# Kernel tuning notes

Hardware: AMD Instinct MI355X
Metric: run time of the kernel (lower is better)

Reference implementation:

```python
import jax, jax.numpy as jnp
import numpy as np
import math

# ---- dims ----
B, N, IN_DIM = 4, 512, 128
D, H, DH = 256, 8, 32          # embed_dim, heads, dim_head
L = 8                           # performer depth
M = int(DH * math.log(DH))      # 110 FAVOR+ random features (performer_pytorch default)
HID = 256                       # lstm hidden
FF = 4 * D
EPS_K = 1e-4                    # kernel feature eps
EPS_D = 1e-6                    # denominator eps


def setup_inputs() -> dict:
    key = jax.random.key(0)
    ks = iter(jax.random.split(key, 40))
    def nrm(shape, s=0.02):
        return jax.random.normal(next(ks), shape, dtype=jnp.float32) * s
    z = lambda shape: jnp.zeros(shape, jnp.float32)
    o = lambda shape: jnp.ones(shape, jnp.float32)
    return {
        "x": jax.random.normal(next(ks), (B, N, IN_DIM), dtype=jnp.float32),
        # input projection
        "Win_w": nrm((D, IN_DIM)), "Win_b": z((D,)),
        # performer layers (stacked over L)
        "ln1_w": o((L, D)), "ln1_b": z((L, D)),
        "Wq": nrm((L, D, D)), "bq": z((L, D)),
        "Wk": nrm((L, D, D)), "bk": z((L, D)),
        "Wv": nrm((L, D, D)), "bv": z((L, D)),
        "Wo": nrm((L, D, D)), "bo": z((L, D)),
        "proj": jax.random.normal(next(ks), (L, M, DH), dtype=jnp.float32),  # FAVOR+ projections
        "ln2_w": o((L, D)), "ln2_b": z((L, D)),
        "Wff1": nrm((L, FF, D)), "bff1": z((L, FF)),
        "Wff2": nrm((L, D, FF)), "bff2": z((L, D)),
        # BiLSTM: layer0 input D, layers1-2 input 2*HID; [dir] / [layer,dir] stacks
        "Wih0": nrm((2, 4 * HID, D)), "Whh0": nrm((2, 4 * HID, HID)), "b0": z((2, 2, 4 * HID)),
        "Wih12": nrm((2, 2, 4 * HID, 2 * HID)), "Whh12": nrm((2, 2, 4 * HID, HID)), "b12": z((2, 2, 2, 4 * HID)),
        # final head
        "fc_w": nrm((1, 2 * HID)), "fc_b": z((1,)),
    }


def layer_norm(x, w, b):
    mu = jnp.mean(x, -1, keepdims=True)
    var = jnp.mean((x - mu) ** 2, -1, keepdims=True)
    return (x - mu) * jax.lax.rsqrt(var + 1e-5) * w + b


def softmax_features(x, proj, is_query):
    # FAVOR+ positive softmax-kernel features. x:[b,h,n,dh], proj:[m,dh]
    xd = x * (DH ** -0.25)
    dd = jnp.einsum('bhnd,md->bhnm', xd, proj)
    diag = 0.5 * jnp.sum(xd * xd, -1)[..., None]            # [b,h,n,1]
    if is_query:
        stab = jnp.max(dd, axis=-1, keepdims=True)
    else:
        stab = jnp.max(dd, axis=(-2, -1), keepdims=True)
    return (M ** -0.5) * (jnp.exp(dd - diag - stab) + EPS_K)


def causal_linear_attention(qp, kp, v):
    # qp,kp:[b,h,n,m], v:[b,h,n,dv] -> [b,h,n,dv]; cumulative-sum causal form
    k_cum = jnp.cumsum(kp, axis=2)
    d_inv = 1.0 / (jnp.einsum('bhnm,bhnm->bhn', qp, k_cum) + EPS_D)
    ctx = jnp.cumsum(jnp.einsum('bhnm,bhnd->bhnmd', kp, v), axis=2)
    return jnp.einsum('bhnmd,bhnm,bhn->bhnd', ctx, qp, d_inv)


def performer_block(x, p):
    (lw1, lb1, wq, bq_, wk, bk_, wv, bv_, wo, bo_, pr, lw2, lb2, w1, b1, w2, b2) = p
    b, n = x.shape[0], x.shape[1]
    y = layer_norm(x, lw1, lb1)
    sh = lambda t: t.reshape(b, n, H, DH).transpose(0, 2, 1, 3)
    q = sh(y @ wq.T + bq_)
    k = sh(y @ wk.T + bk_)
    v = sh(y @ wv.T + bv_)
    qp = softmax_features(q, pr, True)
    kp = softmax_features(k, pr, False)
    o = causal_linear_attention(qp, kp, v)
    o = o.transpose(0, 2, 1, 3).reshape(b, n, D)
    x = x + o @ wo.T + bo_
    y = layer_norm(x, lw2, lb2)
    x = x + jax.nn.gelu(y @ w1.T + b1, approximate=False) @ w2.T + b2
    return x, None


def lstm_dir(x, wih, whh, b, reverse):
    # x:[B,N,in] -> hs:[B,N,HID]; torch gate order i,f,g,o
    xs = jnp.flip(x, 1) if reverse else x
    gi = xs.transpose(1, 0, 2) @ wih.T + b                  # [N,B,4H] precomputed input part
    def step(carry, g_in):
        h, c = carry
        g = g_in + h @ whh.T
        i, f, gg, oo = jnp.split(g, 4, axis=-1)
        c = jax.nn.sigmoid(f) * c + jax.nn.sigmoid(i) * jnp.tanh(gg)
        h = jax.nn.sigmoid(oo) * jnp.tanh(c)
        return (h, c), h
    h0 = jnp.zeros((x.shape[0], HID), x.dtype)
    _, hs = jax.lax.scan(step, (h0, h0), gi)
    hs = hs.transpose(1, 0, 2)
    return jnp.flip(hs, 1) if reverse else hs


def bilstm_layer(x, wih, whh, b):
    fwd = lstm_dir(x, wih[0], whh[0], b[0, 0] + b[0, 1], False)
    bwd = lstm_dir(x, wih[1], whh[1], b[1, 0] + b[1, 1], True)
    return jnp.concatenate([fwd, bwd], -1)


def reference(x, Win_w, Win_b, ln1_w, ln1_b, Wq, bq, Wk, bk, Wv, bv, Wo, bo, proj,
              ln2_w, ln2_b, Wff1, bff1, Wff2, bff2,
              Wih0, Whh0, b0, Wih12, Whh12, b12, fc_w, fc_b):
    h = x @ Win_w.T + Win_b
    params = (ln1_w, ln1_b, Wq, bq, Wk, bk, Wv, bv, Wo, bo, proj, ln2_w, ln2_b, Wff1, bff1, Wff2, bff2)
    h, _ = jax.lax.scan(performer_block, h, params)       # 8 performer layers
    # dropout is identity at eval
    h = bilstm_layer(h, Wih0, Whh0, b0)
    h = bilstm_layer(h, Wih12[0], Whh12[0], b12[0])
    h = bilstm_layer(h, Wih12[1], Whh12[1], b12[1])
    return h[:, -1, :] @ fc_w.T + fc_b                    # [B,1]
```

## Files before the change

### kernel.cpp

```cpp
#include <hip/hip_runtime.h>
#include <math.h>

#define B_    4
#define N_    512
#define D_    256
#define H_    8
#define DH_   32
#define M_    110
#define MP_   112
#define FF_   1024
#define HID_  256
#define ROWS_ 2048
#define CHUNK 32
#define NCH   16

#define OFF_H      0u
#define OFF_Y      524288u
#define OFF_Q      1048576u
#define OFF_K      1572864u
#define OFF_V      2097152u
#define OFF_O      2621440u
#define OFF_FF     3145728u
#define OFF_QP     5242880u
#define OFF_KP     7077888u
#define OFF_S      8912896u
#define OFF_MB     9437184u
#define OFF_P      10747904u
#define OFF_KSUM   12582912u
#define OFF_PK     12640256u
#define OFF_DIAG   12697600u
#define OFF_KMAX   12713984u

#define SCALE_X 0.42044820762685725f
#define SCALE_M 0.09534625892455924f

__device__ __forceinline__ float sigmoidf_(float x){ return 1.0f/(1.0f+expf(-x)); }
__device__ __forceinline__ float geluf_(float x){ return 0.5f*x*(1.0f+erff(x*0.70710678118654752f)); }
__device__ __forceinline__ unsigned encf_(float x){ unsigned u=__float_as_uint(x); return (u&0x80000000u)?~u:(u|0x80000000u); }
__device__ __forceinline__ float decf_(unsigned u){ return (u&0x80000000u)?__uint_as_float(u&0x7fffffffu):__uint_as_float(~u); }

typedef unsigned u32x4_ __attribute__((ext_vector_type(4)));

__device__ __forceinline__ u32x4_ ld4_l2_(const unsigned* p){
  u32x4_ v;
  asm volatile("global_load_dwordx4 %0, %1, off sc0\n\ts_waitcnt vmcnt(0)"
               : "=v"(v) : "v"(p));
  return v;
}
__device__ __forceinline__ u32x4_ ld4_far_(const unsigned* p){
  u32x4_ v;
  asm volatile("global_load_dwordx4 %0, %1, off sc0 sc1\n\ts_waitcnt vmcnt(0)"
               : "=v"(v) : "v"(p));
  return v;
}

__global__ __launch_bounds__(256) void gemm_k(
    const float* __restrict__ A, const float* __restrict__ W,
    const float* __restrict__ b1, const float* __restrict__ b2,
    const float* __restrict__ R, float* __restrict__ C,
    int M, int N, int K, int act)
{
  __shared__ float As[16][72];
  __shared__ float Ws[16][72];
  const int tid = threadIdx.x;
  const int tx = tid & 15, ty = tid >> 4;
  const int i0 = blockIdx.y * 64, j0 = blockIdx.x * 64;
  const int lr = tid >> 2, lc = (tid & 3) << 2;
  float acc[4][4] = {};
  for (int k0 = 0; k0 < K; k0 += 16) {
    float4 a4 = *(const float4*)(A + (size_t)(i0 + lr) * K + k0 + lc);
    float4 w4 = *(const float4*)(W + (size_t)(j0 + lr) * K + k0 + lc);
    __syncthreads();
    As[lc+0][lr]=a4.x; As[lc+1][lr]=a4.y; As[lc+2][lr]=a4.z; As[lc+3][lr]=a4.w;
    Ws[lc+0][lr]=w4.x; Ws[lc+1][lr]=w4.y; Ws[lc+2][lr]=w4.z; Ws[lc+3][lr]=w4.w;
    __syncthreads();
    #pragma unroll
    for (int kk = 0; kk < 16; kk++) {
      float4 av = *(const float4*)&As[kk][ty*4];
      float4 wv = *(const float4*)&Ws[kk][tx*4];
      acc[0][0] += av.x*wv.x; acc[0][1] += av.x*wv.y; acc[0][2] += av.x*wv.z; acc[0][3] += av.x*wv.w;
      acc[1][0] += av.y*wv.x; acc[1][1] += av.y*wv.y; acc[1][2] += av.y*wv.z; acc[1][3] += av.y*wv.w;
      acc[2][0] += av.z*wv.x; acc[2][1] += av.z*wv.y; acc[2][2] += av.z*wv.z; acc[2][3] += av.z*wv.w;
      acc[3][0] += av.w*wv.x; acc[3][1] += av.w*wv.y; acc[3][2] += av.w*wv.z; acc[3][3] += av.w*wv.w;
    }
  }
  #pragma unroll
  for (int ii = 0; ii < 4; ii++) {
    int gi_ = i0 + ty*4 + ii;
    #pragma unroll
    for (int jj = 0; jj < 4; jj++) {
      int gj = j0 + tx*4 + jj;
      float v = acc[ii][jj];
      if (b1) v += b1[gj];
      if (b2) v += b2[gj];
      if (act) v = geluf_(v);
      if (R) v += R[(size_t)gi_ * N + gj];
      C[(size_t)gi_ * N + gj] = v;
    }
  }
}

__global__ __launch_bounds__(256) void gemm3_k(
    const float* __restrict__ A,
    const float* __restrict__ W0, const float* __restrict__ W1, const float* __restrict__ W2,
    const float* __restrict__ c0_, const float* __restrict__ c1_, const float* __restrict__ c2_,
    float* __restrict__ O0, float* __restrict__ O1, float* __restrict__ O2)
{
  const int which = blockIdx.x >> 2;
  const float* W  = which == 0 ? W0 : which == 1 ? W1 : W2;
  const float* bb = which == 0 ? c0_ : which == 1 ? c1_ : c2_;
  float* C        = which == 0 ? O0 : which == 1 ? O1 : O2;
  __shared__ float As[16][72];
  __shared__ float Ws[16][72];
  const int tid = threadIdx.x;
  const int tx = tid & 15, ty = tid >> 4;
  const int i0 = blockIdx.y * 64, j0 = (blockIdx.x & 3) * 64;
  const int lr = tid >> 2, lc = (tid & 3) << 2;
  float acc[4][4] = {};
  for (int k0 = 0; k0 < 256; k0 += 16) {
    float4 a4 = *(const float4*)(A + (size_t)(i0 + lr) * 256 + k0 + lc);
    float4 w4 = *(const float4*)(W + (size_t)(j0 + lr) * 256 + k0 + lc);
    __syncthreads();
    As[lc+0][lr]=a4.x; As[lc+1][lr]=a4.y; As[lc+2][lr]=a4.z; As[lc+3][lr]=a4.w;
    Ws[lc+0][lr]=w4.x; Ws[lc+1][lr]=w4.y; Ws[lc+2][lr]=w4.z; Ws[lc+3][lr]=w4.w;
    __syncthreads();
    #pragma unroll
    for (int kk = 0; kk < 16; kk++) {
      float4 av = *(const float4*)&As[kk][ty*4];
      float4 wv = *(const float4*)&Ws[kk][tx*4];
      acc[0][0] += av.x*wv.x; acc[0][1] += av.x*wv.y; acc[0][2] += av.x*wv.z; acc[0][3] += av.x*wv.w;
      acc[1][0] += av.y*wv.x; acc[1][1] += av.y*wv.y; acc[1][2] += av.y*wv.z; acc[1][3] += av.y*wv.w;
      acc[2][0] += av.z*wv.x; acc[2][1] += av.z*wv.y; acc[2][2] += av.z*wv.z; acc[2][3] += av.z*wv.w;
      acc[3][0] += av.w*wv.x; acc[3][1] += av.w*wv.y; acc[3][2] += av.w*wv.z; acc[3][3] += av.w*wv.w;
    }
  }
  #pragma unroll
  for (int ii = 0; ii < 4; ii++) {
    int gi_ = i0 + ty*4 + ii;
    #pragma unroll
    for (int jj = 0; jj < 4; jj++) {
      int gj = j0 + tx*4 + jj;
      C[(size_t)gi_ * 256 + gj] = acc[ii][jj] + bb[gj];
    }
  }
}

__global__ __launch_bounds__(256) void ln_k(const float* __restrict__ x, const float* __restrict__ w,
                                            const float* __restrict__ b, float* __restrict__ y)
{
  const int row = blockIdx.x, t = threadIdx.x;
  float v = x[(size_t)row * 256 + t];
  float s = v;
  #pragma unroll
  for (int o = 32; o >= 1; o >>= 1) s += __shfl_xor(s, o, 64);
  __shared__ float w1_[4], w2_[4];
  const int wid = t >> 6, lane = t & 63;
  if (lane == 0) w1_[wid] = s;
  __syncthreads();
  float mu = (w1_[0] + w1_[1] + w1_[2] + w1_[3]) * (1.0f/256.0f);
  float d = v - mu;
  float s2 = d * d;
  #pragma unroll
  for (int o = 32; o >= 1; o >>= 1) s2 += __shfl_xor(s2, o, 64);
  if (lane == 0) w2_[wid] = s2;
  __syncthreads();
  float var = (w2_[0] + w2_[1] + w2_[2] + w2_[3]) * (1.0f/256.0f);
  y[(size_t)row * 256 + t] = d * (1.0f / sqrtf(var + 1e-5f)) * w[t] + b[t];
}

__global__ __launch_bounds__(256) void featq_k(const float* __restrict__ q, const float* __restrict__ proj,
                                               float* __restrict__ qp)
{
  const int wid = threadIdx.x >> 6, lane = threadIdx.x & 63;
  const int p = blockIdx.x * 4 + wid;
  const int bh = p >> 9, n = p & 511;
  const int b = bh >> 3, h = bh & 7;
  __shared__ float xs[4][32];
  const float* qrow = q + ((size_t)(b * N_ + n)) * D_ + h * DH_;
  if (lane < 32) xs[wid][lane] = qrow[lane] * SCALE_X;
  __syncthreads();
  float diag = 0.f;
  #pragma unroll
  for (int d = 0; d < 32; d++) { float xv = xs[wid][d]; diag += xv * xv; }
  diag *= 0.5f;
  const int m0 = lane, m1 = 64 + lane;
  float dd0 = 0.f, dd1 = -INFINITY;
  #pragma unroll
  for (int d = 0; d < 32; d++) dd0 += xs[wid][d] * proj[m0 * 32 + d];
  if (m1 < M_) {
    float a = 0.f;
    #pragma unroll
    for (int d = 0; d < 32; d++) a += xs[wid][d] * proj[m1 * 32 + d];
    dd1 = a;
  }
  float mx = fmaxf(dd0, dd1);
  #pragma unroll
  for (int o = 32; o >= 1; o >>= 1) mx = fmaxf(mx, __shfl_xor(mx, o, 64));
  float* out = qp + (size_t)p * MP_;
  out[m0] = SCALE_M * (expf(dd0 - diag - mx) + 1e-4f);
  if (m1 < M_)        out[m1] = SCALE_M * (expf(dd1 - diag - mx) + 1e-4f);
  else if (m1 < MP_)  out[m1] = 0.f;
}

__global__ __launch_bounds__(256) void featk1_k(const float* __restrict__ k, const float* __restrict__ proj,
                                                float* __restrict__ kpraw, float* __restrict__ diagb,
                                                unsigned* __restrict__ kmax)
{
  const int wid = threadIdx.x >> 6, lane = threadIdx.x & 63;
  const int p = blockIdx.x * 4 + wid;
  const int bh = p >> 9, n = p & 511;
  const int b = bh >> 3, h = bh & 7;
  __shared__ float xs[4][32];
  const float* krow = k + ((size_t)(b * N_ + n)) * D_ + h * DH_;
  if (lane < 32) xs[wid][lane] = krow[lane] * SCALE_X;
  __syncthreads();
  float diag = 0.f;
  #pragma unroll
  for (int d = 0; d < 32; d++) { float xv = xs[wid][d]; diag += xv * xv; }
  diag *= 0.5f;
  const int m0 = lane, m1 = 64 + lane;
  float dd0 = 0.f, dd1 = -INFINITY;
  #pragma unroll
  for (int d = 0; d < 32; d++) dd0 += xs[wid][d] * proj[m0 * 32 + d];
  if (m1 < M_) {
    float a = 0.f;
    #pragma unroll
    for (int d = 0; d < 32; d++) a += xs[wid][d] * proj[m1 * 32 + d];
    dd1 = a;
  }
  float mx = fmaxf(dd0, dd1);
  #pragma unroll
  for (int o = 32; o >= 1; o >>= 1) mx = fmaxf(mx, __shfl_xor(mx, o, 64));
  float* out = kpraw + (size_t)p * MP_;
  out[m0] = dd0;
  if (m1 < M_) out[m1] = dd1;
  if (lane == 0) { diagb[p] = diag; atomicMax(kmax + bh, encf_(mx)); }
}

__global__ __launch_bounds__(256) void featk2_k(float* __restrict__ kp, const float* __restrict__ diagb,
                                                const unsigned* __restrict__ kmax)
{
  const int idx = blockIdx.x * 256 + threadIdx.x;
  const int p = idx / MP_, m = idx - p * MP_;
  const int bh = p >> 9;
  float v = 0.f;
  if (m < M_) v = SCALE_M * (expf(kp[idx] - diagb[p] - decf_(kmax[bh])) + 1e-4f);
  kp[idx] = v;
}

__global__ __launch_bounds__(256) void csum_k(const float* __restrict__ kp, const float* __restrict__ v,
                                              float* __restrict__ S, float* __restrict__ ksum)
{
  const int bh = blockIdx.x >> 4, c = blockIdx.x & 15;
  const int b = bh >> 3, h = bh & 7;
  __shared__ float kpc[CHUNK * MP_];
  __shared__ float vc[CHUNK][DH_];
  const float* kpbase = kp + ((size_t)bh * N_ + c * CHUNK) * MP_;
  for (int f = threadIdx.x; f < CHUNK * MP_; f += 256) kpc[f] = kpbase[f];
  for (int f = threadIdx.x; f < CHUNK * DH_; f += 256) {
    int i = f >> 5, d = f & 31;
    vc[i][d] = v[((size_t)(b * N_ + c * CHUNK + i)) * D_ + h * DH_ + d];
  }
  __syncthreads();
  const int d = threadIdx.x & 31, mg = threadIdx.x >> 5;
  float Sa[14] = {};
  for (int i = 0; i < CHUNK; i++) {
    float vv = vc[i][d];
    #pragma unroll
    for (int j = 0; j < 14; j++) Sa[j] += kpc[i * MP_ + mg * 14 + j] * vv;
  }
  float* Sout = S + (((size_t)blockIdx.x) * MP_ + mg * 14) * DH_ + d;
  #pragma unroll
  for (int j = 0; j < 14; j++) Sout[(size_t)j * DH_] = Sa[j];
  if (threadIdx.x < MP_) {
    float s = 0.f;
    for (int i = 0; i < CHUNK; i++) s += kpc[i * MP_ + threadIdx.x];
    ksum[(size_t)blockIdx.x * MP_ + threadIdx.x] = s;
  }
}

__global__ __launch_bounds__(256) void cpref_k(const float* __restrict__ S, const float* __restrict__ ksum,
                                               float* __restrict__ P, float* __restrict__ pk)
{
  const int bh = blockIdx.x;
  const int d = threadIdx.x & 31, mg = threadIdx.x >> 5;
  float run[14] = {};
  for (int c = 0; c < NCH; c++) {
    size_t base = (((size_t)(bh * NCH + c)) * MP_ + mg * 14) * DH_ + d;
    #pragma unroll
    for (int j = 0; j < 14; j++) { P[base + (size_t)j * DH_] = run[j]; run[j] += S[base + (size_t)j * DH_]; }
  }
  if (threadIdx.x < MP_) {
    float r = 0.f;
    for (int c = 0; c < NCH; c++) {
      size_t o = (size_t)(bh * NCH + c) * MP_ + threadIdx.x;
      pk[o] = r; r += ksum[o];
    }
  }
}

__global__ __launch_bounds__(256, 1) void attn_k(const float* __restrict__ qp, const float* __restrict__ kp,
                                                 const float* __restrict__ v, const float* __restrict__ P,
                                                 const float* __restrict__ pk, float* __restrict__ o)
{
  const int bh = blockIdx.x >> 4, c = blockIdx.x & 15;
  const int b = bh >> 3, h = bh & 7;
  __shared__ float qpc[CHUNK * 113];
  __shared__ float kpc[CHUNK * 113];
  __shared__ float vc[CHUNK][DH_];
  __shared__ float Pl[MP_ * DH_];
  __shared__ float pkl[MP_];
  __shared__ float Al[CHUNK * 33];
  __shared__ float den[CHUNK];
  const int t = threadIdx.x;
  const float* qbase = qp + ((size_t)bh * N_ + c * CHUNK) * MP_;
  const float* kbase = kp + ((size_t)bh * N_ + c * CHUNK) * MP_;
  for (int f = t; f < CHUNK * MP_; f += 256) {
    int i = f / MP_, m = f - i * MP_;
    qpc[i * 113 + m] = qbase[f];
    kpc[i * 113 + m] = kbase[f];
  }
  for (int f = t; f < CHUNK * DH_; f += 256) {
    int i = f >> 5, d = f & 31;
    vc[i][d] = v[((size_t)(b * N_ + c * CHUNK + i)) * D_ + h * DH_ + d];
  }
  for (int f = t; f < MP_ * DH_; f += 256) Pl[f] = P[((size_t)blockIdx.x) * MP_ * DH_ + f];
  if (t < MP_) pkl[t] = pk[(size_t)blockIdx.x * MP_ + t];
  __syncthreads();
  {
    const int ti = t >> 4, tj = t & 15;
    float a00 = 0.f, a01 = 0.f, a10 = 0.f, a11 = 0.f;
    for (int m = 0; m < MP_; m++) {
      float q0 = qpc[(ti*2+0)*113 + m], q1 = qpc[(ti*2+1)*113 + m];
      float k0 = kpc[(tj*2+0)*113 + m], k1 = kpc[(tj*2+1)*113 + m];
      a00 += q0*k0; a01 += q0*k1; a10 += q1*k0; a11 += q1*k1;
    }
    const int i0_ = ti*2, j0_ = tj*2;
    Al[(i0_  )*33 + j0_  ] = (j0_   <= i0_  ) ? a00 : 0.f;
    Al[(i0_  )*33 + j0_+1] = (j0_+1 <= i0_  ) ? a01 : 0.f;
    Al[(i0_+1)*33 + j0_  ] = (j0_   <= i0_+1) ? a10 : 0.f;
    Al[(i0_+1)*33 + j0_+1] = (j0_+1 <= i0_+1) ? a11 : 0.f;
  }
  __syncthreads();
  if (t < CHUNK) {
    const int i = t; float s = 0.f;
    for (int m = 0; m < MP_; m++) s += qpc[i*113 + m] * pkl[m];
    for (int j = 0; j <= i; j++) s += Al[i*33 + j];
    den[i] = 1.0f / (s + 1e-6f);
  }
  __syncthreads();
  {
    const int d = t & 31, ig = t >> 5;
    float Pd[MP_];
    #pragma unroll
    for (int m = 0; m < MP_; m++) Pd[m] = Pl[m * DH_ + d];
    float vd[CHUNK];
    #pragma unroll
    for (int j = 0; j < CHUNK; j++) vd[j] = vc[j][d];
    for (int r = 0; r < 4; r++) {
      const int i = ig * 4 + r;
      float acc = 0.f;
      #pragma unroll
      for (int m = 0; m < MP_; m++) acc += qpc[i*113 + m] * Pd[m];
      #pragma unroll
      for (int j = 0; j < CHUNK; j++) acc += Al[i*33 + j] * vd[j];
      o[((size_t)(b * N_ + c * CHUNK + i)) * D_ + h * DH_ + d] = acc * den[i];
    }
  }
}

__global__ __launch_bounds__(256, 1) void rec_k(
    const float* __restrict__ gi, const float* __restrict__ whh,
    float* __restrict__ hs, float* __restrict__ hx)
{
  const int bid = blockIdx.x;
  if ((bid & 7) > 1) return;
  const int dir = bid & 7;
  const int s = bid >> 3;
  if (s >= 16) return;
  const int t = threadIdx.x;

  const float* giD = gi + (size_t)dir * 2097152;
  const float* whD = whh + (size_t)dir * 262144;
  float* hxD = hx + (size_t)dir * 524288;

  __shared__ __align__(16) float h_sh[4][256];
  __shared__ __align__(16) float red[64 * 33];
  __shared__ __align__(16) float gsh[64 * 5];

  __builtin_amdgcn_fence(__ATOMIC_ACQUIRE, "agent");

  const int rg = t & 31, kq = t >> 5;
  float4 w4[2][8];
  #pragma unroll
  for (int rr = 0; rr < 2; rr++) {
    const int rho = rg * 2 + rr;
    const int grow = (rho >> 4) * 256 + s * 16 + (rho & 15);
    const float4* src = (const float4*)(whD + (size_t)grow * 256 + kq * 32);
    #pragma unroll
    for (int q = 0; q < 8; q++) w4[rr][q] = src[q];
  }

  const int rho2 = t & 63, b2 = t >> 6;
  const float* pgi = giD + (size_t)b2 * 524288 + (size_t)((rho2 >> 4) * 256 + s * 16 + (rho2 & 15));

  ((float4*)h_sh)[t] = make_float4(0.f, 0.f, 0.f, 0.f);
  float c0 = 0.f;
  __syncthreads();

  int n = dir ? 511 : 0;
  float gnext = pgi[(size_t)n * 1024];

  for (int step = 0; step < 512; step++) {
    const float gval = gnext;
    const int n2 = dir ? (510 - step) : (step + 1);
    if (step < 511) gnext = pgi[(size_t)n2 * 1024];

    float acc[2][4] = {};
    #pragma unroll
    for (int q = 0; q < 8; q++) {
      float4 h0 = *(const float4*)&h_sh[0][kq * 32 + q * 4];
      float4 h1 = *(const float4*)&h_sh[1][kq * 32 + q * 4];
      float4 h2 = *(const float4*)&h_sh[2][kq * 32 + q * 4];
      float4 h3 = *(const float4*)&h_sh[3][kq * 32 + q * 4];
      #pragma unroll
      for (int rr = 0; rr < 2; rr++) {
        float4 w = w4[rr][q];
        acc[rr][0] += w.x*h0.x + w.y*h0.y + w.z*h0.z + w.w*h0.w;
        acc[rr][1] += w.x*h1.x + w.y*h1.y + w.z*h1.z + w.w*h1.w;
        acc[rr][2] += w.x*h2.x + w.y*h2.y + w.z*h2.z + w.w*h2.w;
        acc[rr][3] += w.x*h3.x + w.y*h3.y + w.z*h3.z + w.w*h3.w;
      }
    }
    #pragma unroll
    for (int rr = 0; rr < 2; rr++)
      #pragma unroll
      for (int b = 0; b < 4; b++)
        red[(rg * 2 + rr) * 33 + b * 8 + kq] = acc[rr][b];
    __syncthreads();

    {
      float pre = gval;
      #pragma unroll
      for (int q = 0; q < 8; q++) pre += red[rho2 * 33 + b2 * 8 + q];
      gsh[rho2 * 5 + b2] = pre;
    }
    __syncthreads();

    if (t < 64) {
      const int j = t & 15, bb = t >> 4;
      const float iv = gsh[(0 * 16 + j) * 5 + bb];
      const float fv = gsh[(1 * 16 + j) * 5 + bb];
      const float gg = gsh[(2 * 16 + j) * 5 + bb];
      const float ov = gsh[(3 * 16 + j) * 5 + bb];
      c0 = sigmoidf_(fv) * c0 + sigmoidf_(iv) * tanhf(gg);
      const float hv = sigmoidf_(ov) * tanhf(c0);
      hs[(size_t)(bb * 512 + n) * 512 + dir * 256 + s * 16 + j] = hv;
      if (step < 511)
        __hip_atomic_store(hxD + (size_t)step * 1024 + bb * 256 + s * 16 + j, hv,
                           __ATOMIC_RELAXED, __HIP_MEMORY_SCOPE_AGENT);
    }

    if (step < 511) {
      const unsigned* srcp = (const unsigned*)(hxD + (size_t)step * 1024) + t * 4;
      u32x4_ v = ld4_l2_(srcp);
      int it = 0;
      while (v.x == 0xFFFFFFFFu || v.y == 0xFFFFFFFFu ||
             v.z == 0xFFFFFFFFu || v.w == 0xFFFFFFFFu) {
        v = ((++it) & 1) ? ld4_far_(srcp) : ld4_l2_(srcp);
      }
      float4 hv4;
      hv4.x = __uint_as_float(v.x); hv4.y = __uint_as_float(v.y);
      hv4.z = __uint_as_float(v.z); hv4.w = __uint_as_float(v.w);
      ((float4*)h_sh)[t] = hv4;
      __syncthreads();
    }
    n = n2;
  }
}

__global__ __launch_bounds__(256) void fc_k(const float* __restrict__ hs, const float* __restrict__ fw,
                                            const float* __restrict__ fb, float* __restrict__ out)
{
  const int t = threadIdx.x;
  float p[4] = {};
  for (int j = t; j < 512; j += 256) {
    const float w = fw[j];
    #pragma unroll
    for (int b = 0; b < 4; b++) p[b] += hs[(size_t)(b * 512 + 511) * 512 + j] * w;
  }
  #pragma unroll
  for (int b = 0; b < 4; b++)
    #pragma unroll
    for (int o = 32; o >= 1; o >>= 1) p[b] += __shfl_xor(p[b], o, 64);
  __shared__ float r4[4][4];
  const int wid = t >> 6, lane = t & 63;
  if (lane == 0) {
    #pragma unroll
    for (int b = 0; b < 4; b++) r4[b][wid] = p[b];
  }
  __syncthreads();
  if (t == 0) {
    #pragma unroll
    for (int b = 0; b < 4; b++) out[b] = r4[b][0] + r4[b][1] + r4[b][2] + r4[b][3] + fb[0];
  }
}

extern "C" void kernel_launch(void* const* d_in, const int* in_sizes, int n_in,
                              void* d_out, int out_size, void* d_ws, size_t ws_size,
                              hipStream_t stream) {
  (void)in_sizes; (void)n_in; (void)out_size; (void)ws_size;
  const float* x     = (const float*)d_in[0];
  const float* Win_w = (const float*)d_in[1];
  const float* Win_b = (const float*)d_in[2];
  const float* ln1w  = (const float*)d_in[3];
  const float* ln1b  = (const float*)d_in[4];
  const float* Wq    = (const float*)d_in[5];
  const float* bq    = (const float*)d_in[6];
  const float* Wk    = (const float*)d_in[7];
  const float* bk    = (const float*)d_in[8];
  const float* Wv    = (const float*)d_in[9];
  const float* bv    = (const float*)d_in[10];
  const float* Wo    = (const float*)d_in[11];
  const float* bo    = (const float*)d_in[12];
  const float* proj  = (const float*)d_in[13];
  const float* ln2w  = (const float*)d_in[14];
  const float* ln2b  = (const float*)d_in[15];
  const float* Wff1  = (const float*)d_in[16];
  const float* bff1  = (const float*)d_in[17];
  const float* Wff2  = (const float*)d_in[18];
  const float* bff2  = (const float*)d_in[19];
  const float* Wih0  = (const float*)d_in[20];
  const float* Whh0  = (const float*)d_in[21];
  const float* b0    = (const float*)d_in[22];
  const float* Wih12 = (const float*)d_in[23];
  const float* Whh12 = (const float*)d_in[24];
  const float* b12   = (const float*)d_in[25];
  const float* fcw   = (const float*)d_in[26];
  const float* fcb   = (const float*)d_in[27];

  float* ws = (float*)d_ws;
  float* H   = ws + OFF_H;
  float* Y   = ws + OFF_Y;
  float* Q   = ws + OFF_Q;
  float* Kb  = ws + OFF_K;
  float* V   = ws + OFF_V;
  float* O   = ws + OFF_O;
  float* FFb = ws + OFF_FF;
  float* QP  = ws + OFF_QP;
  float* KP  = ws + OFF_KP;
  float* S   = ws + OFF_S;
  float* P   = ws + OFF_P;
  float* KS  = ws + OFF_KSUM;
  float* PK  = ws + OFF_PK;
  float* DG  = ws + OFF_DIAG;
  unsigned* KMAX = (unsigned*)(ws + OFF_KMAX);
  float* GI  = ws + OFF_QP;
  float* MB  = ws + OFF_MB;
  float* BLa = ws + OFF_FF;
  float* BLb = ws + OFF_FF + 1048576;

  const dim3 blk(256);
  const dim3 g256(4, 32);
  const dim3 g768(12, 32);
  const dim3 g1024(16, 32);

  gemm_k<<<g256, blk, 0, stream>>>(x, Win_w, Win_b, nullptr, nullptr, H, ROWS_, 256, 128, 0);

  for (int l = 0; l < 8; l++) {
    const float* prj = proj + (size_t)l * 3520;
    ln_k<<<ROWS_, blk, 0, stream>>>(H, ln1w + l*256, ln1b + l*256, Y);
    gemm3_k<<<g768, blk, 0, stream>>>(Y, Wq + (size_t)l*65536, Wk + (size_t)l*65536, Wv + (size_t)l*65536,
                                      bq + l*256, bk + l*256, bv + l*256, Q, Kb, V);
    (void)hipMemsetAsync(KMAX, 0, 32 * sizeof(unsigned), stream);
    featq_k<<<4096, blk, 0, stream>>>(Q, prj, QP);
    featk1_k<<<4096, blk, 0, stream>>>(Kb, prj, KP, DG, KMAX);
    featk2_k<<<7168, blk, 0, stream>>>(KP, DG, KMAX);
    csum_k<<<512, blk, 0, stream>>>(KP, V, S, KS);
    cpref_k<<<32, blk, 0, stream>>>(S, KS, P, PK);
    attn_k<<<512, blk, 0, stream>>>(QP, KP, V, P, PK, O);
    gemm_k<<<g256, blk, 0, stream>>>(O, Wo + (size_t)l*65536, bo + l*256, nullptr, H, H, ROWS_, 256, 256, 0);
    ln_k<<<ROWS_, blk, 0, stream>>>(H, ln2w + l*256, ln2b + l*256, Y);
    gemm_k<<<g1024, blk, 0, stream>>>(Y, Wff1 + (size_t)l*262144, bff1 + l*1024, nullptr, nullptr, FFb, ROWS_, 1024, 256, 1);
    gemm_k<<<g256, blk, 0, stream>>>(FFb, Wff2 + (size_t)l*262144, bff2 + l*256, nullptr, H, H, ROWS_, 256, 1024, 0);
  }

  (void)hipMemsetAsync(MB, 0xFF, 3145728u * sizeof(float), stream);

  gemm_k<<<g1024, blk, 0, stream>>>(H, Wih0,          b0,        b0 + 1024, nullptr, GI,           ROWS_, 1024, 256, 0);
  gemm_k<<<g1024, blk, 0, stream>>>(H, Wih0 + 262144, b0 + 2048, b0 + 3072, nullptr, GI + 2097152, ROWS_, 1024, 256, 0);
  rec_k<<<128, blk, 0, stream>>>(GI, Whh0, BLa, MB);

  gemm_k<<<g1024, blk, 0, stream>>>(BLa, Wih12,          b12,        b12 + 1024, nullptr, GI,           ROWS_, 1024, 512, 0);
  gemm_k<<<g1024, blk, 0, stream>>>(BLa, Wih12 + 524288, b12 + 2048, b12 + 3072, nullptr, GI + 2097152, ROWS_, 1024, 512, 0);
  rec_k<<<128, blk, 0, stream>>>(GI, Whh12, BLb, MB + 1048576);

  gemm_k<<<g1024, blk, 0, stream>>>(BLb, Wih12 + 1048576, b12 + 4096, b12 + 5120, nullptr, GI,           ROWS_, 1024, 512, 0);
  gemm_k<<<g1024, blk, 0, stream>>>(BLb, Wih12 + 1572864, b12 + 6144, b12 + 7168, nullptr, GI + 2097152, ROWS_, 1024, 512, 0);
  rec_k<<<128, blk, 0, stream>>>(GI, Whh12 + 524288, BLa, MB + 2097152);

  fc_k<<<1, blk, 0, stream>>>(BLa, fcw, fcb, (float*)d_out);
}
```

Measured before the change: 6.891 ms.

## Fuse feature kernels, fold key exp into consumers, merge LSTM gate GEMMs, dual mailboxes

Merges the query and key feature kernels into a single launch and drops the separate key-normalisation pass. The exp normalisation of the raw key features is now recomputed inside csum_k and attn_k as they load them. The two per-direction input-gate GEMMs of each LSTM layer become one launch with both biases summed in. The recurrent kernel now publishes each hidden state to two mailbox buffers, one written with an L2-scoped store and one with an agent-scope atomic, and polls the L2 copy mostly and the far copy only occasionally, to cut cross-CU handoff latency; an empty asm is also added around the Whh loads. This adds extra memsets, reuses the Y/K workspace regions as mailboxes, and the exp work is now done twice, once in each consumer.

```diff
diff --git a/kernel.cpp b/kernel.cpp
--- a/kernel.cpp
+++ b/kernel.cpp
@@ -53,6 +53,9 @@
                : "=v"(v) : "v"(p));
   return v;
 }
+__device__ __forceinline__ void st_l2_(float* p, float x){
+  asm volatile("global_store_dword %0, %1, off sc0" :: "v"(p), "v"(x) : "memory");
+}
 
 __global__ __launch_bounds__(256) void gemm_k(
     const float* __restrict__ A, const float* __restrict__ W,
@@ -145,6 +148,50 @@
   }
 }
 
+__global__ __launch_bounds__(256) void gemmgi_k(
+    const float* __restrict__ A, const float* __restrict__ W, const float* __restrict__ bvec,
+    float* __restrict__ C, int K, int wGap, int bGap)
+{
+  const int dir = blockIdx.x >> 4;
+  const float* Wd = W + (size_t)dir * wGap;
+  const float* b1 = bvec + (size_t)dir * bGap;
+  const float* b2 = b1 + 1024;
+  float* Cd = C + (size_t)dir * 2097152;
+  __shared__ float As[16][72];
+  __shared__ float Ws[16][72];
+  const int tid = threadIdx.x;
+  const int tx = tid & 15, ty = tid >> 4;
+  const int i0 = blockIdx.y * 64, j0 = (blockIdx.x & 15) * 64;
+  const int lr = tid >> 2, lc = (tid & 3) << 2;
+  float acc[4][4] = {};
+  for (int k0 = 0; k0 < K; k0 += 16) {
+    float4 a4 = *(const float4*)(A + (size_t)(i0 + lr) * K + k0 + lc);
+    float4 w4 = *(const float4*)(Wd + (size_t)(j0 + lr) * K + k0 + lc);
+    __syncthreads();
+    As[lc+0][lr]=a4.x; As[lc+1][lr]=a4.y; As[lc+2][lr]=a4.z; As[lc+3][lr]=a4.w;
+    Ws[lc+0][lr]=w4.x; Ws[lc+1][lr]=w4.y; Ws[lc+2][lr]=w4.z; Ws[lc+3][lr]=w4.w;
+    __syncthreads();
+    #pragma unroll
+    for (int kk = 0; kk < 16; kk++) {
+      float4 av = *(const float4*)&As[kk][ty*4];
+      float4 wv = *(const float4*)&Ws[kk][tx*4];
+      acc[0][0] += av.x*wv.x; acc[0][1] += av.x*wv.y; acc[0][2] += av.x*wv.z; acc[0][3] += av.x*wv.w;
+      acc[1][0] += av.y*wv.x; acc[1][1] += av.y*wv.y; acc[1][2] += av.y*wv.z; acc[1][3] += av.y*wv.w;
+      acc[2][0] += av.z*wv.x; acc[2][1] += av.z*wv.y; acc[2][2] += av.z*wv.z; acc[2][3] += av.z*wv.w;
+      acc[3][0] += av.w*wv.x; acc[3][1] += av.w*wv.y; acc[3][2] += av.w*wv.z; acc[3][3] += av.w*wv.w;
+    }
+  }
+  #pragma unroll
+  for (int ii = 0; ii < 4; ii++) {
+    int gi_ = i0 + ty*4 + ii;
+    #pragma unroll
+    for (int jj = 0; jj < 4; jj++) {
+      int gj = j0 + tx*4 + jj;
+      Cd[(size_t)gi_ * 1024 + gj] = acc[ii][jj] + b1[gj] + b2[gj];
+    }
+  }
+}
+
 __global__ __launch_bounds__(256) void ln_k(const float* __restrict__ x, const float* __restrict__ w,
                                             const float* __restrict__ b, float* __restrict__ y)
 {
@@ -168,16 +215,20 @@
   y[(size_t)row * 256 + t] = d * (1.0f / sqrtf(var + 1e-5f)) * w[t] + b[t];
 }
 
-__global__ __launch_bounds__(256) void featq_k(const float* __restrict__ q, const float* __restrict__ proj,
-                                               float* __restrict__ qp)
-{
+__global__ __launch_bounds__(256) void feat_k(const float* __restrict__ q, const float* __restrict__ kk,
+                                              const float* __restrict__ proj,
+                                              float* __restrict__ qp, float* __restrict__ kpraw,
+                                              float* __restrict__ diagb, unsigned* __restrict__ kmax)
+{
+  const int isq = (blockIdx.x < 4096);
+  const int bx = isq ? blockIdx.x : (blockIdx.x - 4096);
   const int wid = threadIdx.x >> 6, lane = threadIdx.x & 63;
-  const int p = blockIdx.x * 4 + wid;
+  const int p = bx * 4 + wid;
   const int bh = p >> 9, n = p & 511;
   const int b = bh >> 3, h = bh & 7;
   __shared__ float xs[4][32];
-  const float* qrow = q + ((size_t)(b * N_ + n)) * D_ + h * DH_;
-  if (lane < 32) xs[wid][lane] = qrow[lane] * SCALE_X;
+  const float* xrow = (isq ? q : kk) + ((size_t)(b * N_ + n)) * D_ + h * DH_;
+  if (lane < 32) xs[wid][lane] = xrow[lane] * SCALE_X;
   __syncthreads();
   float diag = 0.f;
   #pragma unroll
@@ -196,59 +247,21 @@
   float mx = fmaxf(dd0, dd1);
   #pragma unroll
   for (int o = 32; o >= 1; o >>= 1) mx = fmaxf(mx, __shfl_xor(mx, o, 64));
-  float* out = qp + (size_t)p * MP_;
-  out[m0] = SCALE_M * (expf(dd0 - diag - mx) + 1e-4f);
-  if (m1 < M_)        out[m1] = SCALE_M * (expf(dd1 - diag - mx) + 1e-4f);
-  else if (m1 < MP_)  out[m1] = 0.f;
-}
-
-__global__ __launch_bounds__(256) void featk1_k(const float* __restrict__ k, const float* __restrict__ proj,
-                                                float* __restrict__ kpraw, float* __restrict__ diagb,
-                                                unsigned* __restrict__ kmax)
-{
-  const int wid = threadIdx.x >> 6, lane = threadIdx.x & 63;
-  const int p = blockIdx.x * 4 + wid;
-  const int bh = p >> 9, n = p & 511;
-  const int b = bh >> 3, h = bh & 7;
-  __shared__ float xs[4][32];
-  const float* krow = k + ((size_t)(b * N_ + n)) * D_ + h * DH_;
-  if (lane < 32) xs[wid][lane] = krow[lane] * SCALE_X;
-  __syncthreads();
-  float diag = 0.f;
-  #pragma unroll
-  for (int d = 0; d < 32; d++) { float xv = xs[wid][d]; diag += xv * xv; }
-  diag *= 0.5f;
-  const int m0 = lane, m1 = 64 + lane;
-  float dd0 = 0.f, dd1 = -INFINITY;
-  #pragma unroll
-  for (int d = 0; d < 32; d++) dd0 += xs[wid][d] * proj[m0 * 32 + d];
-  if (m1 < M_) {
-    float a = 0.f;
-    #pragma unroll
-    for (int d = 0; d < 32; d++) a += xs[wid][d] * proj[m1 * 32 + d];
-    dd1 = a;
-  }
-  float mx = fmaxf(dd0, dd1);
-  #pragma unroll
-  for (int o = 32; o >= 1; o >>= 1) mx = fmaxf(mx, __shfl_xor(mx, o, 64));
-  float* out = kpraw + (size_t)p * MP_;
-  out[m0] = dd0;
-  if (m1 < M_) out[m1] = dd1;
-  if (lane == 0) { diagb[p] = diag; atomicMax(kmax + bh, encf_(mx)); }
-}
-
-__global__ __launch_bounds__(256) void featk2_k(float* __restrict__ kp, const float* __restrict__ diagb,
-                                                const unsigned* __restrict__ kmax)
-{
-  const int idx = blockIdx.x * 256 + threadIdx.x;
-  const int p = idx / MP_, m = idx - p * MP_;
-  const int bh = p >> 9;
-  float v = 0.f;
-  if (m < M_) v = SCALE_M * (expf(kp[idx] - diagb[p] - decf_(kmax[bh])) + 1e-4f);
-  kp[idx] = v;
+  if (isq) {
+    float* out = qp + (size_t)p * MP_;
+    out[m0] = SCALE_M * (expf(dd0 - diag - mx) + 1e-4f);
+    if (m1 < M_)        out[m1] = SCALE_M * (expf(dd1 - diag - mx) + 1e-4f);
+    else if (m1 < MP_)  out[m1] = 0.f;
+  } else {
+    float* out = kpraw + (size_t)p * MP_;
+    out[m0] = dd0;
+    if (m1 < M_) out[m1] = dd1;
+    if (lane == 0) { diagb[p] = diag; atomicMax(kmax + bh, encf_(mx)); }
+  }
 }
 
 __global__ __launch_bounds__(256) void csum_k(const float* __restrict__ kp, const float* __restrict__ v,
+                                              const float* __restrict__ diagb, const unsigned* __restrict__ kmax,
                                               float* __restrict__ S, float* __restrict__ ksum)
 {
   const int bh = blockIdx.x >> 4, c = blockIdx.x & 15;
@@ -256,7 +269,15 @@
   __shared__ float kpc[CHUNK * MP_];
   __shared__ float vc[CHUNK][DH_];
   const float* kpbase = kp + ((size_t)bh * N_ + c * CHUNK) * MP_;
-  for (int f = threadIdx.x; f < CHUNK * MP_; f += 256) kpc[f] = kpbase[f];
+  const float kmx = decf_(kmax[bh]);
+  const int r0 = bh * N_ + c * CHUNK;
+  for (int f = threadIdx.x; f < CHUNK * MP_; f += 256) {
+    int i = f / MP_, m = f - i * MP_;
+    float raw = kpbase[f];
+    float val = 0.f;
+    if (m < M_) val = SCALE_M * (expf(raw - diagb[r0 + i] - kmx) + 1e-4f);
+    kpc[f] = val;
+  }
   for (int f = threadIdx.x; f < CHUNK * DH_; f += 256) {
     int i = f >> 5, d = f & 31;
     vc[i][d] = v[((size_t)(b * N_ + c * CHUNK + i)) * D_ + h * DH_ + d];
@@ -301,7 +322,9 @@
 
 __global__ __launch_bounds__(256, 1) void attn_k(const float* __restrict__ qp, const float* __restrict__ kp,
                                                  const float* __restrict__ v, const float* __restrict__ P,
-                                                 const float* __restrict__ pk, float* __restrict__ o)
+                                                 const float* __restrict__ pk,
+                                                 const float* __restrict__ diagb, const unsigned* __restrict__ kmax,
+                                                 float* __restrict__ o)
 {
   const int bh = blockIdx.x >> 4, c = blockIdx.x & 15;
   const int b = bh >> 3, h = bh & 7;
@@ -315,10 +338,15 @@
   const int t = threadIdx.x;
   const float* qbase = qp + ((size_t)bh * N_ + c * CHUNK) * MP_;
   const float* kbase = kp + ((size_t)bh * N_ + c * CHUNK) * MP_;
+  const float kmx = decf_(kmax[bh]);
+  const int r0 = bh * N_ + c * CHUNK;
   for (int f = t; f < CHUNK * MP_; f += 256) {
     int i = f / MP_, m = f - i * MP_;
     qpc[i * 113 + m] = qbase[f];
-    kpc[i * 113 + m] = kbase[f];
+    float raw = kbase[f];
+    float val = 0.f;
+    if (m < M_) val = SCALE_M * (expf(raw - diagb[r0 + i] - kmx) + 1e-4f);
+    kpc[i * 113 + m] = val;
   }
   for (int f = t; f < CHUNK * DH_; f += 256) {
     int i = f >> 5, d = f & 31;
@@ -371,7 +399,7 @@
 
 __global__ __launch_bounds__(256, 1) void rec_k(
     const float* __restrict__ gi, const float* __restrict__ whh,
-    float* __restrict__ hs, float* __restrict__ hx)
+    float* __restrict__ hs, float* __restrict__ hxa, float* __restrict__ hxb)
 {
   const int bid = blockIdx.x;
   if ((bid & 7) > 1) return;
@@ -382,7 +410,8 @@
 
   const float* giD = gi + (size_t)dir * 2097152;
   const float* whD = whh + (size_t)dir * 262144;
-  float* hxD = hx + (size_t)dir * 524288;
+  float* hxaD = hxa + (size_t)dir * 524288;
+  float* hxbD = hxb + (size_t)dir * 524288;
 
   __shared__ __align__(16) float h_sh[4][256];
   __shared__ __align__(16) float red[64 * 33];
@@ -398,7 +427,11 @@
     const int grow = (rho >> 4) * 256 + s * 16 + (rho & 15);
     const float4* src = (const float4*)(whD + (size_t)grow * 256 + kq * 32);
     #pragma unroll
-    for (int q = 0; q < 8; q++) w4[rr][q] = src[q];
+    for (int q = 0; q < 8; q++) {
+      float4 tmp = src[q];
+      asm("" : "+v"(tmp.x), "+v"(tmp.y), "+v"(tmp.z), "+v"(tmp.w));
+      w4[rr][q] = tmp;
+    }
   }
 
   const int rho2 = t & 63, b2 = t >> 6;
@@ -456,18 +489,23 @@
       c0 = sigmoidf_(fv) * c0 + sigmoidf_(iv) * tanhf(gg);
       const float hv = sigmoidf_(ov) * tanhf(c0);
       hs[(size_t)(bb * 512 + n) * 512 + dir * 256 + s * 16 + j] = hv;
-      if (step < 511)
-        __hip_atomic_store(hxD + (size_t)step * 1024 + bb * 256 + s * 16 + j, hv,
-                           __ATOMIC_RELAXED, __HIP_MEMORY_SCOPE_AGENT);
+      if (step < 511) {
+        const size_t off = (size_t)step * 1024 + bb * 256 + s * 16 + j;
+        st_l2_(hxaD + off, hv);
+        __hip_atomic_store(hxbD + off, hv, __ATOMIC_RELAXED,
+                           __HIP_MEMORY_SCOPE_AGENT);
+      }
     }
 
     if (step < 511) {
-      const unsigned* srcp = (const unsigned*)(hxD + (size_t)step * 1024) + t * 4;
-      u32x4_ v = ld4_l2_(srcp);
+      const unsigned* pa = (const unsigned*)(hxaD + (size_t)step * 1024) + t * 4;
+      const unsigned* pb = (const unsigned*)(hxbD + (size_t)step * 1024) + t * 4;
+      u32x4_ v = ld4_l2_(pa);
       int it = 0;
       while (v.x == 0xFFFFFFFFu || v.y == 0xFFFFFFFFu ||
              v.z == 0xFFFFFFFFu || v.w == 0xFFFFFFFFu) {
-        v = ((++it) & 1) ? ld4_far_(srcp) : ld4_l2_(srcp);
+        ++it;
+        v = ((it & 3) == 3) ? ld4_far_(pb) : ld4_l2_(pa);
       }
       float4 hv4;
       hv4.x = __uint_as_float(v.x); hv4.y = __uint_as_float(v.y);
@@ -556,7 +594,9 @@
   float* DG  = ws + OFF_DIAG;
   unsigned* KMAX = (unsigned*)(ws + OFF_KMAX);
   float* GI  = ws + OFF_QP;
-  float* MB  = ws + OFF_MB;
+  float* MA  = ws + OFF_MB;
+  float* MB0 = ws + OFF_Y;
+  float* MB1 = ws + OFF_K;
   float* BLa = ws + OFF_FF;
   float* BLb = ws + OFF_FF + 1048576;
 
@@ -564,6 +604,7 @@
   const dim3 g256(4, 32);
   const dim3 g768(12, 32);
   const dim3 g1024(16, 32);
+  const dim3 g2048(32, 32);
 
   gemm_k<<<g256, blk, 0, stream>>>(x, Win_w, Win_b, nullptr, nullptr, H, ROWS_, 256, 128, 0);
 
@@ -573,31 +614,28 @@
     gemm3_k<<<g768, blk, 0, stream>>>(Y, Wq + (size_t)l*65536, Wk + (size_t)l*65536, Wv + (size_t)l*65536,
                                       bq + l*256, bk + l*256, bv + l*256, Q, Kb, V);
     (void)hipMemsetAsync(KMAX, 0, 32 * sizeof(unsigned), stream);
-    featq_k<<<4096, blk, 0, stream>>>(Q, prj, QP);
-    featk1_k<<<4096, blk, 0, stream>>>(Kb, prj, KP, DG, KMAX);
-    featk2_k<<<7168, blk, 0, stream>>>(KP, DG, KMAX);
-    csum_k<<<512, blk, 0, stream>>>(KP, V, S, KS);
+    feat_k<<<8192, blk, 0, stream>>>(Q, Kb, prj, QP, KP, DG, KMAX);
+    csum_k<<<512, blk, 0, stream>>>(KP, V, DG, KMAX, S, KS);
     cpref_k<<<32, blk, 0, stream>>>(S, KS, P, PK);
-    attn_k<<<512, blk, 0, stream>>>(QP, KP, V, P, PK, O);
+    attn_k<<<512, blk, 0, stream>>>(QP, KP, V, P, PK, DG, KMAX, O);
     gemm_k<<<g256, blk, 0, stream>>>(O, Wo + (size_t)l*65536, bo + l*256, nullptr, H, H, ROWS_, 256, 256, 0);
     ln_k<<<ROWS_, blk, 0, stream>>>(H, ln2w + l*256, ln2b + l*256, Y);
     gemm_k<<<g1024, blk, 0, stream>>>(Y, Wff1 + (size_t)l*262144, bff1 + l*1024, nullptr, nullptr, FFb, ROWS_, 1024, 256, 1);
     gemm_k<<<g256, blk, 0, stream>>>(FFb, Wff2 + (size_t)l*262144, bff2 + l*256, nullptr, H, H, ROWS_, 256, 1024, 0);
   }
 
-  (void)hipMemsetAsync(MB, 0xFF, 3145728u * sizeof(float), stream);
-
-  gemm_k<<<g1024, blk, 0, stream>>>(H, Wih0,          b0,        b0 + 1024, nullptr, GI,           ROWS_, 1024, 256, 0);
-  gemm_k<<<g1024, blk, 0, stream>>>(H, Wih0 + 262144, b0 + 2048, b0 + 3072, nullptr, GI + 2097152, ROWS_, 1024, 256, 0);
-  rec_k<<<128, blk, 0, stream>>>(GI, Whh0, BLa, MB);
-
-  gemm_k<<<g1024, blk, 0, stream>>>(BLa, Wih12,          b12,        b12 + 1024, nullptr, GI,           ROWS_, 1024, 512, 0);
-  gemm_k<<<g1024, blk, 0, stream>>>(BLa, Wih12 + 524288, b12 + 2048, b12 + 3072, nullptr, GI + 2097152, ROWS_, 1024, 512, 0);
-  rec_k<<<128, blk, 0, stream>>>(GI, Whh12, BLb, MB + 1048576);
-
-  gemm_k<<<g1024, blk, 0, stream>>>(BLb, Wih12 + 1048576, b12 + 4096, b12 + 5120, nullptr, GI,           ROWS_, 1024, 512, 0);
-  gemm_k<<<g1024, blk, 0, stream>>>(BLb, Wih12 + 1572864, b12 + 6144, b12 + 7168, nullptr, GI + 2097152, ROWS_, 1024, 512, 0);
-  rec_k<<<128, blk, 0, stream>>>(GI, Whh12 + 524288, BLa, MB + 2097152);
+  (void)hipMemsetAsync(MA, 0xFF, 3145728u * sizeof(float), stream);
+  (void)hipMemsetAsync(MB0, 0xFF, 2097152u * sizeof(float), stream);
+
+  gemmgi_k<<<g2048, blk, 0, stream>>>(H, Wih0, b0, GI, 256, 262144, 2048);
+  rec_k<<<128, blk, 0, stream>>>(GI, Whh0, BLa, MA, MB0);
+  (void)hipMemsetAsync(MB0, 0xFF, 1048576u * sizeof(float), stream);
+
+  gemmgi_k<<<g2048, blk, 0, stream>>>(BLa, Wih12, b12, GI, 512, 524288, 2048);
+  rec_k<<<128, blk, 0, stream>>>(GI, Whh12, BLb, MA + 1048576, MB1);
+
+  gemmgi_k<<<g2048, blk, 0, stream>>>(BLb, Wih12 + 1048576, b12 + 4096, GI, 512, 524288, 2048);
+  rec_k<<<128, blk, 0, stream>>>(GI, Whh12 + 524288, BLa, MA + 2097152, MB0);
 
   fc_k<<<1, blk, 0, stream>>>(BLa, fcw, fcb, (float*)d_out);
 }
```

After: 6.811 ms. About the same (-1.2%).
